# Optimization experiments

Measured on AMD Instinct MI355X. Metric: run time of the kernel, lower is better.

The kernel has to match this reference:

```python
import jax, jax.numpy as jnp
import numpy as np

D_MODEL = 2048
D_FF = 8192
BATCH = 4
SEQ = 2048
MAX_EXP = 4
NUM_BITS = 8
C_CHUNKS = 2
SCALE = 0.1


def _pow2_ternary(key, out_dim, in_dim, max_exp):
    """Weights are t * 2^{-e}: ternary sign times power-of-two magnitude."""
    k1, k2 = jax.random.split(key)
    t = jax.random.randint(k1, (out_dim, in_dim), -1, 2).astype(jnp.float32)
    e = jax.random.randint(k2, (out_dim, in_dim), 0, max_exp + 1).astype(jnp.float32)
    return t * jnp.exp2(-e)


def setup_inputs() -> dict:
    key = jax.random.key(0)
    kx, k1, k2 = jax.random.split(key, 3)
    x = jax.random.normal(kx, (BATCH, SEQ, D_MODEL), dtype=jnp.float32)
    W1 = _pow2_ternary(k1, D_FF, D_MODEL, MAX_EXP)   # [d_ff, d_model] torch-style
    W2 = _pow2_ternary(k2, D_MODEL, D_FF, MAX_EXP)   # [d_model, d_ff]
    return {"x": x, "W1": W1, "W2": W2}


def _lookup_act(h):
    # 16-bit (num_bits * c) fixed-point quantize, then table-valued GELU.
    total_bits = NUM_BITS * C_CHUNKS
    qmax = 2 ** (total_bits - 1) - 1
    qmin = -(2 ** (total_bits - 1))
    q = jnp.clip(jnp.round(h / SCALE), qmin, qmax)
    return jax.nn.gelu(q * SCALE)


def reference(x, W1, W2):
    # fc1: [b,s,d_model] x [d_ff,d_model]^T -> [b,s,d_ff]
    h = jnp.einsum('bsd,fd->bsf', x, W1)
    a = _lookup_act(h)
    # fc2: [b,s,d_ff] x [d_model,d_ff]^T -> [b,s,d_model]
    return jnp.einsum('bsf,df->bsd', a, W2)
```

## Files before the change

kernel.cpp:

```cpp
#include <hip/hip_runtime.h>
#include <cstdint>
#include <cstddef>


typedef __bf16 bf16_t;
typedef bf16_t bf16x8 __attribute__((ext_vector_type(8)));
typedef float  floatx4 __attribute__((ext_vector_type(4)));

#define AS1 __attribute__((address_space(1)))
#define AS3 __attribute__((address_space(3)))

__device__ __forceinline__ void async_cp16(const void* g, void* l) {
    __builtin_amdgcn_global_load_lds((const AS1 void*)g, (AS3 void*)l, 16, 0, 0);
}

__device__ __forceinline__ float gelu_fast(float x) {
    const float C0 = 1.5957691216057308f;
    const float C1 = 0.0713548163f;
    float u2 = x * fmaf(C1, x * x, C0);
    float e  = __expf(u2);
    float r  = __builtin_amdgcn_rcpf(1.0f + e);
    return x * (1.0f - r);
}

__global__ __launch_bounds__(256)
void cvt_pack_swz(const float* __restrict__ src, bf16_t* __restrict__ dst,
                  int K, int tshift)
{
    const size_t   oc = (size_t)blockIdx.x * 256 + threadIdx.x;
    const uint32_t ho = ((uint32_t)oc & 1023u) * 16u;
    const size_t   region = oc >> 10;
    const int      h  = (int)(region & 1);
    const size_t   pt = region >> 1;
    const int      t  = (int)(pt & ((1u << tshift) - 1));
    const size_t   p  = pt >> tshift;
    const uint32_t L = ho ^ (((ho >> 9) & 1u) << 5);
    const int      s = (int)(L >> 10);
    const uint32_t u = L & 1023u;
    const size_t   row = p * 256 + (size_t)(h * 128 + (s >> 1) * 16 + (int)(u >> 6));
    const int      k   = (t << 6) + (s & 1) * 32 + (int)((u & 63u) >> 1);
    const float* sp = src + row * (size_t)K + k;
    float4 a = *(const float4*)sp;
    float4 b = *(const float4*)(sp + 4);
    bf16x8 o;
    o[0] = (bf16_t)a.x; o[1] = (bf16_t)a.y; o[2] = (bf16_t)a.z; o[3] = (bf16_t)a.w;
    o[4] = (bf16_t)b.x; o[5] = (bf16_t)b.y; o[6] = (bf16_t)b.z; o[7] = (bf16_t)b.w;
    *(bf16x8*)(dst + oc * 8) = o;
}

template<bool ACT, typename OutT>
__global__ __launch_bounds__(512, 2)
void gemm256(const bf16_t* __restrict__ A, const bf16_t* __restrict__ B,
             OutT* __restrict__ C, int M, int N, int K, int nbxs)
{
    __shared__ __align__(16) bf16_t lds[65536];
    char* const ldsb = (char*)lds;

    const int NT  = K >> 6;
    const int id  = blockIdx.x;
    const int nwg = gridDim.x;
    const int sw = (id & 7) * (nwg >> 3) + (id >> 3);
    const int by = sw >> nbxs;
    const int bx = sw & ((1 << nbxs) - 1);

    const int tid  = threadIdx.x;
    const int lane = tid & 63;
    const int wave = tid >> 6;
    const int wm = wave >> 2;
    const int wn = wave & 3;

    const bf16_t* const Ap = A + (size_t)by * NT * 16384;
    const bf16_t* const Bp = B + (size_t)bx * NT * 16384;

    uint32_t lsw = (uint32_t)(((lane & 15) << 6) + ((lane >> 4) << 4));
    lsw ^= ((lsw >> 9) & 1u) << 5;

    const uint32_t aBase = (uint32_t)(2 + wm) << 14;
    const uint32_t bBase = (uint32_t)(wn >> 1) << 14;
    const int bSub = (wn & 1) * 4;

    floatx4 acc[8][4];
    #pragma unroll
    for (int i = 0; i < 8; ++i)
      #pragma unroll
      for (int j = 0; j < 4; ++j)
        acc[i][j] = (floatx4)0.0f;

    auto stage = [&](int t, int j) {
        const bf16_t* g = (j < 2) ? (Bp + (size_t)t * 16384 + (size_t)j * 8192)
                                  : (Ap + (size_t)t * 16384 + (size_t)(j - 2) * 8192);
        char* l = ldsb + (((t & 1) << 16) + (j << 14));
        async_cp16((const char*)g + tid * 16, l + tid * 16);
        async_cp16((const char*)g + 8192 + tid * 16, l + 8192 + tid * 16);
    };

    stage(0, 0); stage(0, 1); stage(0, 2); stage(0, 3);
    stage(1, 0); stage(1, 1); stage(1, 2); stage(1, 3);
    asm volatile("s_waitcnt vmcnt(8)" ::: "memory");
    __builtin_amdgcn_s_barrier();

    bf16x8 b01[2][2], af[4][2];
    {
        const char* bB0 = ldsb + bBase;
        const char* aB0 = ldsb + aBase;
        #pragma unroll
        for (int fn = 0; fn < 2; ++fn)
          #pragma unroll
          for (int ks = 0; ks < 2; ++ks)
            b01[fn][ks] = *(const bf16x8*)(bB0 + (((((bSub + fn) << 1) + ks) << 10) | lsw));
        #pragma unroll
        for (int fm = 0; fm < 4; ++fm)
          #pragma unroll
          for (int ks = 0; ks < 2; ++ks)
            af[fm][ks] = *(const bf16x8*)(aB0 + ((((fm << 1) + ks) << 10) | lsw));
    }

    for (int t = 0; t < NT; ++t) {
        const char* aB  = ldsb + ((t & 1) << 16) + aBase;
        const char* bBc = ldsb + ((t & 1) << 16) + bBase;
        const bool s1 = (t + 1 < NT);
        const bool s2 = (t + 2 < NT);

        bf16x8 b23[2][2];
        #pragma unroll
        for (int fn = 0; fn < 2; ++fn)
          #pragma unroll
          for (int ks = 0; ks < 2; ++ks)
            b23[fn][ks] = *(const bf16x8*)(bBc + (((((bSub + 2 + fn) << 1) + ks) << 10) | lsw));
        __builtin_amdgcn_s_setprio(1);
        #pragma unroll
        for (int ks = 0; ks < 2; ++ks)
          #pragma unroll
          for (int fm = 0; fm < 4; ++fm)
            #pragma unroll
            for (int fn = 0; fn < 2; ++fn)
              acc[fm][fn] = __builtin_amdgcn_mfma_f32_16x16x32_bf16(
                  af[fm][ks], b01[fn][ks], acc[fm][fn], 0, 0, 0);
        __builtin_amdgcn_s_setprio(0);

        asm volatile("s_waitcnt lgkmcnt(0)" ::: "memory");
        __builtin_amdgcn_s_barrier();
        if (s2) { stage(t + 2, 0); stage(t + 2, 1); }
        bf16x8 ah[4][2];
        #pragma unroll
        for (int fm = 0; fm < 4; ++fm)
          #pragma unroll
          for (int ks = 0; ks < 2; ++ks)
            ah[fm][ks] = *(const bf16x8*)(aB + (((((4 + fm) << 1) + ks) << 10) | lsw));
        __builtin_amdgcn_s_setprio(1);
        #pragma unroll
        for (int ks = 0; ks < 2; ++ks)
          #pragma unroll
          for (int fm = 0; fm < 4; ++fm)
            #pragma unroll
            for (int fn = 0; fn < 2; ++fn)
              acc[fm][2 + fn] = __builtin_amdgcn_mfma_f32_16x16x32_bf16(
                  af[fm][ks], b23[fn][ks], acc[fm][2 + fn], 0, 0, 0);
        __builtin_amdgcn_s_setprio(0);

        __builtin_amdgcn_s_setprio(1);
        #pragma unroll
        for (int ks = 0; ks < 2; ++ks)
          #pragma unroll
          for (int fm = 0; fm < 4; ++fm)
            #pragma unroll
            for (int fn = 0; fn < 2; ++fn)
              acc[4 + fm][fn] = __builtin_amdgcn_mfma_f32_16x16x32_bf16(
                  ah[fm][ks], b01[fn][ks], acc[4 + fm][fn], 0, 0, 0);
        __builtin_amdgcn_s_setprio(0);

        if (s2)      asm volatile("s_waitcnt vmcnt(4)" ::: "memory");
        else if (s1) asm volatile("s_waitcnt vmcnt(0)" ::: "memory");
        __builtin_amdgcn_s_barrier();
        if (s1) {
            const char* bBn = ldsb + (((t + 1) & 1) << 16) + bBase;
            const char* aBn = ldsb + (((t + 1) & 1) << 16) + aBase;
            #pragma unroll
            for (int fn = 0; fn < 2; ++fn)
              #pragma unroll
              for (int ks = 0; ks < 2; ++ks)
                b01[fn][ks] = *(const bf16x8*)(bBn + (((((bSub + fn) << 1) + ks) << 10) | lsw));
            #pragma unroll
            for (int fm = 0; fm < 4; ++fm)
              #pragma unroll
              for (int ks = 0; ks < 2; ++ks)
                af[fm][ks] = *(const bf16x8*)(aBn + ((((fm << 1) + ks) << 10) | lsw));
        }
        if (s2) { stage(t + 2, 2); stage(t + 2, 3); }
        __builtin_amdgcn_s_setprio(1);
        #pragma unroll
        for (int ks = 0; ks < 2; ++ks)
          #pragma unroll
          for (int fm = 0; fm < 4; ++fm)
            #pragma unroll
            for (int fn = 0; fn < 2; ++fn)
              acc[4 + fm][2 + fn] = __builtin_amdgcn_mfma_f32_16x16x32_bf16(
                  ah[fm][ks], b23[fn][ks], acc[4 + fm][2 + fn], 0, 0, 0);
        __builtin_amdgcn_s_setprio(0);
    }

    if constexpr (ACT) {
        __syncthreads();
        const uint32_t rbase = (uint32_t)(wn * 2 + wm) << 14;
        #pragma unroll
        for (int fm = 0; fm < 8; ++fm)
          #pragma unroll
          for (int fn = 0; fn < 4; ++fn)
            #pragma unroll
            for (int r = 0; r < 4; ++r) {
                float h = acc[fm][fn][r];
                float q = rintf(h * 10.0f);
                q = fminf(fmaxf(q, -32768.0f), 32767.0f);
                h = gelu_fast(q * 0.1f);
                uint32_t L = ((uint32_t)((fm << 1) + (fn >> 1)) << 10)
                           + (uint32_t)((((lane >> 4) << 2) + r) << 6)
                           + (uint32_t)((((fn & 1) << 4) + (lane & 15)) << 1);
                uint32_t P = L ^ (((L >> 9) & 1u) << 5);
                *(bf16_t*)(ldsb + rbase + P) = (bf16_t)h;
            }
        __syncthreads();
        const int nkt2 = N >> 6;
        bf16_t* const Cb = (bf16_t*)C;
        #pragma unroll
        for (int it = 0; it < 16; ++it) {
            const int ch = it * 512 + tid;
            const int rg = ch >> 10;
            const int c  = ch & 1023;
            const size_t gr = ((size_t)by * nkt2 + (size_t)(bx * 4) + (rg >> 1)) * 2
                            + (size_t)(rg & 1);
            bf16x8 v = *(const bf16x8*)(ldsb + (size_t)ch * 16);
            *(bf16x8*)((char*)Cb + gr * 16384 + (size_t)c * 16) = v;
        }
    } else {
        const int r0 = by * 256 + wm * 128;
        const int c0 = bx * 256 + wn * 64;
        #pragma unroll
        for (int fm = 0; fm < 8; ++fm)
          #pragma unroll
          for (int fn = 0; fn < 4; ++fn) {
            const int col = c0 + fn * 16 + (lane & 15);
            #pragma unroll
            for (int r = 0; r < 4; ++r) {
              const int row = r0 + fm * 16 + ((lane >> 4) << 2) + r;
              C[(size_t)row * N + col] = (OutT)acc[fm][fn][r];
            }
          }
    }
}

extern "C" void kernel_launch(void* const* d_in, const int* in_sizes, int n_in,
                              void* d_out, int out_size, void* d_ws, size_t ws_size,
                              hipStream_t stream)
{
    const int M  = 8192;
    const int DM = 2048;
    const int DF = 8192;

    const float* x  = (const float*)d_in[0];
    const float* W1 = (const float*)d_in[1];
    const float* W2 = (const float*)d_in[2];
    float* out = (float*)d_out;

    bf16_t* xb  = (bf16_t*)d_ws;
    bf16_t* w1b = xb  + (size_t)M  * DM;
    bf16_t* w2b = w1b + (size_t)DF * DM;
    bf16_t* act = w2b + (size_t)DM * DF;

    cvt_pack_swz<<<8192, 256, 0, stream>>>(x,  xb,  DM, 5);
    cvt_pack_swz<<<8192, 256, 0, stream>>>(W1, w1b, DM, 5);
    cvt_pack_swz<<<8192, 256, 0, stream>>>(W2, w2b, DF, 7);

    gemm256<true, bf16_t><<<dim3(1024), 512, 0, stream>>>(xb, w1b, act, M, DF, DM, 5);
    gemm256<false, float><<<dim3(256), 512, 0, stream>>>(act, w2b, out, M, DM, DF, 3);
}
```

Baseline: 661.0 us.

## Load B fragments directly from global memory, halving LDS to A only

B tile fragments are no longer staged through LDS. Each wave reads them straight from global memory in the pre-tiled layout, and only A is double-buffered in LDS, which halves shared memory to 64KB. One barrier per k-step is removed, and the activation epilogue is split into two phases so it fits the smaller LDS. This aims to cut LDS traffic and synchronization and possibly to raise occupancy. The cost is that B loads become direct global/L2 reads on the critical path with waits of vmcnt(0), and B is re-read redundantly by waves that share it.

```diff
diff --git a/kernel.cpp b/kernel.cpp
--- a/kernel.cpp
+++ b/kernel.cpp
@@ -53,7 +53,7 @@
 void gemm256(const bf16_t* __restrict__ A, const bf16_t* __restrict__ B,
              OutT* __restrict__ C, int M, int N, int K, int nbxs)
 {
-    __shared__ __align__(16) bf16_t lds[65536];
+    __shared__ __align__(16) bf16_t lds[32768];
     char* const ldsb = (char*)lds;
 
     const int NT  = K >> 6;
@@ -70,14 +70,19 @@
     const int wn = wave & 3;
 
     const bf16_t* const Ap = A + (size_t)by * NT * 16384;
-    const bf16_t* const Bp = B + (size_t)bx * NT * 16384;
+    const char*  const Bpb = (const char*)(B + (size_t)bx * NT * 16384);
 
     uint32_t lsw = (uint32_t)(((lane & 15) << 6) + ((lane >> 4) << 4));
     lsw ^= ((lsw >> 9) & 1u) << 5;
 
-    const uint32_t aBase = (uint32_t)(2 + wm) << 14;
-    const uint32_t bBase = (uint32_t)(wn >> 1) << 14;
-    const int bSub = (wn & 1) * 4;
+    const uint32_t aBase  = (uint32_t)wm << 14;
+    const uint32_t bHalf  = (uint32_t)(wn >> 1) << 14;
+    const int      bSub   = (wn & 1) * 4;
+
+    auto bfrag = [&](int t, int fn, int ks) -> const bf16x8* {
+        return (const bf16x8*)(Bpb + (size_t)t * 32768 + bHalf
+                               + (uint32_t)((((bSub + fn) << 1) + ks) << 10) + lsw);
+    };
 
     floatx4 acc[8][4];
     #pragma unroll
@@ -86,28 +91,25 @@
       for (int j = 0; j < 4; ++j)
         acc[i][j] = (floatx4)0.0f;
 
-    auto stage = [&](int t, int j) {
-        const bf16_t* g = (j < 2) ? (Bp + (size_t)t * 16384 + (size_t)j * 8192)
-                                  : (Ap + (size_t)t * 16384 + (size_t)(j - 2) * 8192);
-        char* l = ldsb + (((t & 1) << 16) + (j << 14));
+    auto stageA = [&](int t, int j) {
+        const bf16_t* g = Ap + (size_t)t * 16384 + (size_t)j * 8192;
+        char* l = ldsb + (((t & 1) << 15) + (j << 14));
         async_cp16((const char*)g + tid * 16, l + tid * 16);
         async_cp16((const char*)g + 8192 + tid * 16, l + 8192 + tid * 16);
     };
 
-    stage(0, 0); stage(0, 1); stage(0, 2); stage(0, 3);
-    stage(1, 0); stage(1, 1); stage(1, 2); stage(1, 3);
-    asm volatile("s_waitcnt vmcnt(8)" ::: "memory");
+    stageA(0, 0); stageA(0, 1); stageA(1, 0); stageA(1, 1);
+    __builtin_amdgcn_sched_barrier(0);
+    bf16x8 b01[2][2], af[4][2];
+    #pragma unroll
+    for (int fn = 0; fn < 2; ++fn)
+      #pragma unroll
+      for (int ks = 0; ks < 2; ++ks)
+        b01[fn][ks] = *bfrag(0, fn, ks);
+    asm volatile("s_waitcnt vmcnt(0)" ::: "memory");
     __builtin_amdgcn_s_barrier();
-
-    bf16x8 b01[2][2], af[4][2];
     {
-        const char* bB0 = ldsb + bBase;
         const char* aB0 = ldsb + aBase;
-        #pragma unroll
-        for (int fn = 0; fn < 2; ++fn)
-          #pragma unroll
-          for (int ks = 0; ks < 2; ++ks)
-            b01[fn][ks] = *(const bf16x8*)(bB0 + (((((bSub + fn) << 1) + ks) << 10) | lsw));
         #pragma unroll
         for (int fm = 0; fm < 4; ++fm)
           #pragma unroll
@@ -116,8 +118,7 @@
     }
 
     for (int t = 0; t < NT; ++t) {
-        const char* aB  = ldsb + ((t & 1) << 16) + aBase;
-        const char* bBc = ldsb + ((t & 1) << 16) + bBase;
+        const char* aB = ldsb + ((t & 1) << 15) + aBase;
         const bool s1 = (t + 1 < NT);
         const bool s2 = (t + 2 < NT);
 
@@ -126,7 +127,7 @@
         for (int fn = 0; fn < 2; ++fn)
           #pragma unroll
           for (int ks = 0; ks < 2; ++ks)
-            b23[fn][ks] = *(const bf16x8*)(bBc + (((((bSub + 2 + fn) << 1) + ks) << 10) | lsw));
+            b23[fn][ks] = *bfrag(t, 2 + fn, ks);
         __builtin_amdgcn_s_setprio(1);
         #pragma unroll
         for (int ks = 0; ks < 2; ++ks)
@@ -138,9 +139,6 @@
                   af[fm][ks], b01[fn][ks], acc[fm][fn], 0, 0, 0);
         __builtin_amdgcn_s_setprio(0);
 
-        asm volatile("s_waitcnt lgkmcnt(0)" ::: "memory");
-        __builtin_amdgcn_s_barrier();
-        if (s2) { stage(t + 2, 0); stage(t + 2, 1); }
         bf16x8 ah[4][2];
         #pragma unroll
         for (int fm = 0; fm < 4; ++fm)
@@ -169,24 +167,23 @@
                   ah[fm][ks], b01[fn][ks], acc[4 + fm][fn], 0, 0, 0);
         __builtin_amdgcn_s_setprio(0);
 
-        if (s2)      asm volatile("s_waitcnt vmcnt(4)" ::: "memory");
-        else if (s1) asm volatile("s_waitcnt vmcnt(0)" ::: "memory");
-        __builtin_amdgcn_s_barrier();
         if (s1) {
-            const char* bBn = ldsb + (((t + 1) & 1) << 16) + bBase;
-            const char* aBn = ldsb + (((t + 1) & 1) << 16) + aBase;
-            #pragma unroll
-            for (int fn = 0; fn < 2; ++fn)
-              #pragma unroll
-              for (int ks = 0; ks < 2; ++ks)
-                b01[fn][ks] = *(const bf16x8*)(bBn + (((((bSub + fn) << 1) + ks) << 10) | lsw));
+            asm volatile("s_waitcnt vmcnt(0)" ::: "memory");
+            __builtin_amdgcn_s_barrier();
+            if (s2) { stageA(t + 2, 0); stageA(t + 2, 1); }
+            __builtin_amdgcn_sched_barrier(0);
+            const char* aBn = ldsb + (((t + 1) & 1) << 15) + aBase;
             #pragma unroll
             for (int fm = 0; fm < 4; ++fm)
               #pragma unroll
               for (int ks = 0; ks < 2; ++ks)
                 af[fm][ks] = *(const bf16x8*)(aBn + ((((fm << 1) + ks) << 10) | lsw));
+            #pragma unroll
+            for (int fn = 0; fn < 2; ++fn)
+              #pragma unroll
+              for (int ks = 0; ks < 2; ++ks)
+                b01[fn][ks] = *bfrag(t + 1, fn, ks);
         }
-        if (s2) { stage(t + 2, 2); stage(t + 2, 3); }
         __builtin_amdgcn_s_setprio(1);
         #pragma unroll
         for (int ks = 0; ks < 2; ++ks)
@@ -200,36 +197,42 @@
     }
 
     if constexpr (ACT) {
-        __syncthreads();
-        const uint32_t rbase = (uint32_t)(wn * 2 + wm) << 14;
-        #pragma unroll
-        for (int fm = 0; fm < 8; ++fm)
-          #pragma unroll
-          for (int fn = 0; fn < 4; ++fn)
-            #pragma unroll
-            for (int r = 0; r < 4; ++r) {
-                float h = acc[fm][fn][r];
-                float q = rintf(h * 10.0f);
-                q = fminf(fmaxf(q, -32768.0f), 32767.0f);
-                h = gelu_fast(q * 0.1f);
-                uint32_t L = ((uint32_t)((fm << 1) + (fn >> 1)) << 10)
-                           + (uint32_t)((((lane >> 4) << 2) + r) << 6)
-                           + (uint32_t)((((fn & 1) << 4) + (lane & 15)) << 1);
-                uint32_t P = L ^ (((L >> 9) & 1u) << 5);
-                *(bf16_t*)(ldsb + rbase + P) = (bf16_t)h;
-            }
-        __syncthreads();
         const int nkt2 = N >> 6;
         bf16_t* const Cb = (bf16_t*)C;
-        #pragma unroll
-        for (int it = 0; it < 16; ++it) {
-            const int ch = it * 512 + tid;
-            const int rg = ch >> 10;
-            const int c  = ch & 1023;
-            const size_t gr = ((size_t)by * nkt2 + (size_t)(bx * 4) + (rg >> 1)) * 2
-                            + (size_t)(rg & 1);
-            bf16x8 v = *(const bf16x8*)(ldsb + (size_t)ch * 16);
-            *(bf16x8*)((char*)Cb + gr * 16384 + (size_t)c * 16) = v;
+        const uint32_t slot = (uint32_t)(wn * 2 + wm) << 13;
+        #pragma unroll
+        for (int ph = 0; ph < 2; ++ph) {
+            __syncthreads();
+            #pragma unroll
+            for (int f4 = 0; f4 < 4; ++f4) {
+              const int fm = 4 * ph + f4;
+              #pragma unroll
+              for (int fn = 0; fn < 4; ++fn)
+                #pragma unroll
+                for (int r = 0; r < 4; ++r) {
+                    float h = acc[fm][fn][r];
+                    float q = rintf(h * 10.0f);
+                    q = fminf(fmaxf(q, -32768.0f), 32767.0f);
+                    h = gelu_fast(q * 0.1f);
+                    uint32_t L = ((uint32_t)((fm << 1) + (fn >> 1)) << 10)
+                               + (uint32_t)((((lane >> 4) << 2) + r) << 6)
+                               + (uint32_t)((((fn & 1) << 4) + (lane & 15)) << 1);
+                    uint32_t P = (L & 8191u) ^ (((L >> 9) & 1u) << 5);
+                    *(bf16_t*)(ldsb + slot + P) = (bf16_t)h;
+                }
+            }
+            __syncthreads();
+            #pragma unroll
+            for (int it = 0; it < 8; ++it) {
+                const int ch = it * 512 + tid;
+                const int s  = ch >> 9;
+                const int c  = ch & 511;
+                const size_t gr = ((size_t)by * nkt2 + (size_t)(bx * 4)
+                                   + (s >> 1)) * 2 + (size_t)(s & 1);
+                bf16x8 v = *(const bf16x8*)(ldsb + (size_t)ch * 16);
+                *(bf16x8*)((char*)Cb + gr * 16384 + (size_t)ph * 8192
+                           + (size_t)c * 16) = v;
+            }
         }
     } else {
         const int r0 = by * 256 + wm * 128;
```

After: 847.5 us. +28.2%, slower.
